# Kernel optimization log

Measured on AMD Instinct MI355X. Metric: run time of the kernel, lower is better.

## Reference

```python
import jax, jax.numpy as jnp
import numpy as np

NLAG = 300  # int(maxlag/dt) = int(3.0/0.01)


def setup_inputs() -> dict:
    key = jax.random.key(0)
    k1, k2 = jax.random.split(key)
    data1 = jax.random.normal(k1, (64, 32, 3000), dtype=jnp.float32)
    data2 = jax.random.normal(k2, (64, 32, 3000), dtype=jnp.float32)
    return {"data1": data1, "data2": data2}


def reference(data1, data2):
    # Time-domain full cross-correlation via grouped conv1d (PyTorch conv1d
    # does correlation, no kernel flip; lax.conv_general_dilated matches).
    nb, nc, nt = data1.shape
    g = nb * nc
    lhs = data1.reshape(1, g, nt)          # (N=1, C=g, T)
    rhs = data2.reshape(g, 1, nt)          # (O=g, I=1, T) one filter per group
    xcor = jax.lax.conv_general_dilated(
        lhs, rhs,
        window_strides=(1,),
        padding=[(NLAG + 1, NLAG + 1)],
        feature_group_count=g,
        dimension_numbers=("NCH", "OIH", "NCH"),
    )  # (1, g, 2*NLAG+3)
    return xcor.reshape(nb, nc, -1)
```

## Files before the change

### kernel.cpp

```cpp
#include <hip/hip_runtime.h>


#define NT    3000
#define NOUT  603
#define BLOCK 64
#define L1DW  1696
#define L2DW  2048

typedef short bf16x8 __attribute__((ext_vector_type(8)));
typedef float f32x4  __attribute__((ext_vector_type(4)));

static __device__ __forceinline__ uint f2bf(float f) {
    union { float f; uint u; } a; a.f = f;
    return (a.u + 0x7fffu + ((a.u >> 16) & 1u)) >> 16;
}

struct AFrag { uint m1, d0, d1, d2, d3; };

__global__ __launch_bounds__(BLOCK, 2) void xcorr_mfma(
    const float* __restrict__ d1g, const float* __restrict__ d2g,
    float* __restrict__ out)
{
    __shared__ __align__(16) uint l1[L1DW];
    __shared__ __align__(16) uint l2[L2DW];

    const int lane = threadIdx.x & 63;
    const int q = lane >> 4, r = lane & 15;
    const int ch = blockIdx.x;
    const float* __restrict__ g1 = d1g + (size_t)ch * NT;
    const float* __restrict__ g2 = d2g + (size_t)ch * NT;

    for (int j = lane; j < 196; j += BLOCK) {
        const int dw = (j < 152) ? j : 1652 + (j - 152);
        l1[dw] = 0u;
    }
    for (int j = lane; j < 548; j += BLOCK) {
        const int dw = (j < 384) ? j : 1884 + (j - 384);
        l2[dw] = 0u;
    }

    auto stageA = [&](int dstart) {
        const int d = dstart + 4 * lane;
        const int e0 = 2 * (d - 152);
        if (e0 < NT) {
            const float4 v = *(const float4*)(g1 + e0);
            const float4 w = *(const float4*)(g1 + e0 + 4);
            int4 p;
            p.x = (int)(f2bf(v.x) | (f2bf(v.y) << 16));
            p.y = (int)(f2bf(v.z) | (f2bf(v.w) << 16));
            p.z = (int)(f2bf(w.x) | (f2bf(w.y) << 16));
            p.w = (int)(f2bf(w.z) | (f2bf(w.w) << 16));
            *(int4*)(l1 + d) = p;
        }
    };
    auto stageB = [&](int dstart) {
        const int d = dstart + 4 * lane;
        const int e0 = 2 * (d - 384);
        if (e0 < NT) {
            const float4 v = *(const float4*)(g2 + e0);
            const float4 w = *(const float4*)(g2 + e0 + 4);
            int4 p;
            p.x = (int)(f2bf(v.x) | (f2bf(v.y) << 16));
            p.y = (int)(f2bf(v.z) | (f2bf(v.w) << 16));
            p.z = (int)(f2bf(w.x) | (f2bf(w.y) << 16));
            p.w = (int)(f2bf(w.z) | (f2bf(w.w) << 16));
            *(int4*)(l2 + d) = p;
        }
    };

    stageA(152); stageA(408);
    stageB(384); stageB(640);

    int4 fifo[16];
    {
        const int dbP = 256 + 4 * q - 16 * r;
        #pragma unroll
        for (int s = 0; s < 16; ++s)
            fifo[s] = *(const int4*)(l2 + dbP + 16 * s);
    }

    f32x4 a00 = {0.f,0.f,0.f,0.f};
    f32x4 a10 = {0.f,0.f,0.f,0.f};
    f32x4 a01 = {0.f,0.f,0.f,0.f};
    f32x4 a11 = {0.f,0.f,0.f,0.f};

    int da = 130 + 4 * q + r;
    int db = 512 + 4 * q - 16 * r;
    int aPre = 664, bPre = 896;

    auto ldsFetch = [&](int daL, int dbL, AFrag& A, int4& B) {
        const uint* pa = (const uint*)l1 + daL;
        A.m1 = pa[-1]; A.d0 = pa[0]; A.d1 = pa[1]; A.d2 = pa[2]; A.d3 = pa[3];
        B = *(const int4*)((const uint*)l2 + dbL);
    };

    AFrag curA; int4 curB;
    ldsFetch(da, db, curA, curB);
    AFrag nxtA = curA; int4 nxtB = curB;

    for (int c = 0; c < 6; ++c) {
        const int dA = aPre + 4 * lane, eA = 2 * (dA - 152);
        const int dB = bPre + 4 * lane, eB = 2 * (dB - 384);
        const bool okA = eA < NT, okB = eB < NT;
        float4 va0, va1, vb0, vb1;
        if (okA) { va0 = *(const float4*)(g1 + eA); va1 = *(const float4*)(g1 + eA + 4); }
        if (okB) { vb0 = *(const float4*)(g2 + eB); vb1 = *(const float4*)(g2 + eB + 4); }

        #pragma unroll
        for (int u = 0; u < 16; ++u) {
            if (u < 15 || c < 5)
                ldsFetch(da + 16, db + 16, nxtA, nxtB);

            union { uint w[4]; bf16x8 v; int4 i4; } f1, f0, g0, g1u;
            f1.w[0] = curA.d0; f1.w[1] = curA.d1;
            f1.w[2] = curA.d2; f1.w[3] = curA.d3;
            f0.w[0] = (curA.m1 >> 16) | (curA.d0 << 16);
            f0.w[1] = (curA.d0 >> 16) | (curA.d1 << 16);
            f0.w[2] = (curA.d1 >> 16) | (curA.d2 << 16);
            f0.w[3] = (curA.d2 >> 16) | (curA.d3 << 16);

            g0.i4  = curB;
            g1u.i4 = fifo[u];
            fifo[u] = g0.i4;

            a00 = __builtin_amdgcn_mfma_f32_16x16x32_bf16(f0.v, g0.v,  a00, 0, 0, 0);
            a10 = __builtin_amdgcn_mfma_f32_16x16x32_bf16(f1.v, g0.v,  a10, 0, 0, 0);
            a01 = __builtin_amdgcn_mfma_f32_16x16x32_bf16(f0.v, g1u.v, a01, 0, 0, 0);
            a11 = __builtin_amdgcn_mfma_f32_16x16x32_bf16(f1.v, g1u.v, a11, 0, 0, 0);

            curA = nxtA; curB = nxtB;
            da += 16; db += 16;
        }

        if (okA) {
            int4 p;
            p.x = (int)(f2bf(va0.x) | (f2bf(va0.y) << 16));
            p.y = (int)(f2bf(va0.z) | (f2bf(va0.w) << 16));
            p.z = (int)(f2bf(va1.x) | (f2bf(va1.y) << 16));
            p.w = (int)(f2bf(va1.z) | (f2bf(va1.w) << 16));
            *(int4*)(l1 + dA) = p;
        }
        if (okB) {
            int4 p;
            p.x = (int)(f2bf(vb0.x) | (f2bf(vb0.y) << 16));
            p.y = (int)(f2bf(vb0.z) | (f2bf(vb0.w) << 16));
            p.z = (int)(f2bf(vb1.x) | (f2bf(vb1.y) << 16));
            p.w = (int)(f2bf(vb1.z) | (f2bf(vb1.w) << 16));
            *(int4*)(l2 + dB) = p;
        }
        aPre += 256; bPre += 256;
    }

    float* o = out + (size_t)ch * NOUT;
    {
        const int X = 32 * r + 8 * q;
        float4 s0 = {a00[0], a10[0], a00[1], a10[1]};
        float4 s1 = {a00[2], a10[2], a00[3], a10[3]};
        *(float4*)(o + X)     = s0;
        *(float4*)(o + X + 4) = s1;
    }
    {
        const int X = 512 + 32 * r + 8 * q;
        if (X + 7 < NOUT) {
            float4 s0 = {a01[0], a11[0], a01[1], a11[1]};
            float4 s1 = {a01[2], a11[2], a01[3], a11[3]};
            *(float4*)(o + X)     = s0;
            *(float4*)(o + X + 4) = s1;
        } else if (X < NOUT) {
            const float v[8] = {a01[0], a11[0], a01[1], a11[1],
                                a01[2], a11[2], a01[3], a11[3]};
            #pragma unroll
            for (int e = 0; e < 8; ++e)
                if (X + e < NOUT) o[X + e] = v[e];
        }
    }
}

extern "C" void kernel_launch(void* const* d_in, const int* in_sizes, int n_in,
                              void* d_out, int out_size, void* d_ws, size_t ws_size,
                              hipStream_t stream) {
    const float* d1 = (const float*)d_in[0];
    const float* d2 = (const float*)d_in[1];
    float* out = (float*)d_out;
    const int nChannels = in_sizes[0] / NT;
    xcorr_mfma<<<nChannels, BLOCK, 0, stream>>>(d1, d2, out);
}
```

Baseline: 21.89 us.

## Process two channels per wave and prefetch next channel's prologue during compute

Each single-wave block now handles two channels in sequence, cutting the grid from 2048 to 1024 blocks. While the last chunks of the current channel are computing, it loads the next channel's first 1024 samples of both inputs and stages them into LDS regions that have already been consumed. This hides the per-channel prologue load latency behind MFMA work. In exchange there is less block-level parallelism, more registers are live, and the code assumes the channel count is even.

```diff
diff --git a/kernel.cpp b/kernel.cpp
--- a/kernel.cpp
+++ b/kernel.cpp
@@ -4,6 +4,7 @@
 #define NT    3000
 #define NOUT  603
 #define BLOCK 64
+#define CHPW  2
 #define L1DW  1696
 #define L2DW  2048
 
@@ -13,6 +14,15 @@
 static __device__ __forceinline__ uint f2bf(float f) {
     union { float f; uint u; } a; a.f = f;
     return (a.u + 0x7fffu + ((a.u >> 16) & 1u)) >> 16;
+}
+
+static __device__ __forceinline__ int4 pack8(float4 v, float4 w) {
+    int4 p;
+    p.x = (int)(f2bf(v.x) | (f2bf(v.y) << 16));
+    p.y = (int)(f2bf(v.z) | (f2bf(v.w) << 16));
+    p.z = (int)(f2bf(w.x) | (f2bf(w.y) << 16));
+    p.w = (int)(f2bf(w.z) | (f2bf(w.w) << 16));
+    return p;
 }
 
 struct AFrag { uint m1, d0, d1, d2, d3; };
@@ -26,9 +36,7 @@
 
     const int lane = threadIdx.x & 63;
     const int q = lane >> 4, r = lane & 15;
-    const int ch = blockIdx.x;
-    const float* __restrict__ g1 = d1g + (size_t)ch * NT;
-    const float* __restrict__ g2 = d2g + (size_t)ch * NT;
+    const int ch0 = blockIdx.x * CHPW;
 
     for (int j = lane; j < 196; j += BLOCK) {
         const int dw = (j < 152) ? j : 1652 + (j - 152);
@@ -39,140 +47,150 @@
         l2[dw] = 0u;
     }
 
-    auto stageA = [&](int dstart) {
-        const int d = dstart + 4 * lane;
-        const int e0 = 2 * (d - 152);
-        if (e0 < NT) {
-            const float4 v = *(const float4*)(g1 + e0);
-            const float4 w = *(const float4*)(g1 + e0 + 4);
-            int4 p;
-            p.x = (int)(f2bf(v.x) | (f2bf(v.y) << 16));
-            p.y = (int)(f2bf(v.z) | (f2bf(v.w) << 16));
-            p.z = (int)(f2bf(w.x) | (f2bf(w.y) << 16));
-            p.w = (int)(f2bf(w.z) | (f2bf(w.w) << 16));
-            *(int4*)(l1 + d) = p;
-        }
-    };
-    auto stageB = [&](int dstart) {
-        const int d = dstart + 4 * lane;
-        const int e0 = 2 * (d - 384);
-        if (e0 < NT) {
-            const float4 v = *(const float4*)(g2 + e0);
-            const float4 w = *(const float4*)(g2 + e0 + 4);
-            int4 p;
-            p.x = (int)(f2bf(v.x) | (f2bf(v.y) << 16));
-            p.y = (int)(f2bf(v.z) | (f2bf(v.w) << 16));
-            p.z = (int)(f2bf(w.x) | (f2bf(w.y) << 16));
-            p.w = (int)(f2bf(w.z) | (f2bf(w.w) << 16));
-            *(int4*)(l2 + d) = p;
-        }
-    };
-
-    stageA(152); stageA(408);
-    stageB(384); stageB(640);
-
-    int4 fifo[16];
+    const float* g1 = d1g + (size_t)ch0 * NT;
+    const float* g2 = d2g + (size_t)ch0 * NT;
+
     {
-        const int dbP = 256 + 4 * q - 16 * r;
-        #pragma unroll
-        for (int s = 0; s < 16; ++s)
-            fifo[s] = *(const int4*)(l2 + dbP + 16 * s);
-    }
-
-    f32x4 a00 = {0.f,0.f,0.f,0.f};
-    f32x4 a10 = {0.f,0.f,0.f,0.f};
-    f32x4 a01 = {0.f,0.f,0.f,0.f};
-    f32x4 a11 = {0.f,0.f,0.f,0.f};
-
-    int da = 130 + 4 * q + r;
-    int db = 512 + 4 * q - 16 * r;
-    int aPre = 664, bPre = 896;
-
-    auto ldsFetch = [&](int daL, int dbL, AFrag& A, int4& B) {
-        const uint* pa = (const uint*)l1 + daL;
-        A.m1 = pa[-1]; A.d0 = pa[0]; A.d1 = pa[1]; A.d2 = pa[2]; A.d3 = pa[3];
-        B = *(const int4*)((const uint*)l2 + dbL);
-    };
-
-    AFrag curA; int4 curB;
-    ldsFetch(da, db, curA, curB);
-    AFrag nxtA = curA; int4 nxtB = curB;
-
-    for (int c = 0; c < 6; ++c) {
-        const int dA = aPre + 4 * lane, eA = 2 * (dA - 152);
-        const int dB = bPre + 4 * lane, eB = 2 * (dB - 384);
-        const bool okA = eA < NT, okB = eB < NT;
-        float4 va0, va1, vb0, vb1;
-        if (okA) { va0 = *(const float4*)(g1 + eA); va1 = *(const float4*)(g1 + eA + 4); }
-        if (okB) { vb0 = *(const float4*)(g2 + eB); vb1 = *(const float4*)(g2 + eB + 4); }
-
-        #pragma unroll
-        for (int u = 0; u < 16; ++u) {
-            if (u < 15 || c < 5)
-                ldsFetch(da + 16, db + 16, nxtA, nxtB);
-
-            union { uint w[4]; bf16x8 v; int4 i4; } f1, f0, g0, g1u;
-            f1.w[0] = curA.d0; f1.w[1] = curA.d1;
-            f1.w[2] = curA.d2; f1.w[3] = curA.d3;
-            f0.w[0] = (curA.m1 >> 16) | (curA.d0 << 16);
-            f0.w[1] = (curA.d0 >> 16) | (curA.d1 << 16);
-            f0.w[2] = (curA.d1 >> 16) | (curA.d2 << 16);
-            f0.w[3] = (curA.d2 >> 16) | (curA.d3 << 16);
-
-            g0.i4  = curB;
-            g1u.i4 = fifo[u];
-            fifo[u] = g0.i4;
-
-            a00 = __builtin_amdgcn_mfma_f32_16x16x32_bf16(f0.v, g0.v,  a00, 0, 0, 0);
-            a10 = __builtin_amdgcn_mfma_f32_16x16x32_bf16(f1.v, g0.v,  a10, 0, 0, 0);
-            a01 = __builtin_amdgcn_mfma_f32_16x16x32_bf16(f0.v, g1u.v, a01, 0, 0, 0);
-            a11 = __builtin_amdgcn_mfma_f32_16x16x32_bf16(f1.v, g1u.v, a11, 0, 0, 0);
-
-            curA = nxtA; curB = nxtB;
-            da += 16; db += 16;
-        }
-
-        if (okA) {
-            int4 p;
-            p.x = (int)(f2bf(va0.x) | (f2bf(va0.y) << 16));
-            p.y = (int)(f2bf(va0.z) | (f2bf(va0.w) << 16));
-            p.z = (int)(f2bf(va1.x) | (f2bf(va1.y) << 16));
-            p.w = (int)(f2bf(va1.z) | (f2bf(va1.w) << 16));
-            *(int4*)(l1 + dA) = p;
-        }
-        if (okB) {
-            int4 p;
-            p.x = (int)(f2bf(vb0.x) | (f2bf(vb0.y) << 16));
-            p.y = (int)(f2bf(vb0.z) | (f2bf(vb0.w) << 16));
-            p.z = (int)(f2bf(vb1.x) | (f2bf(vb1.y) << 16));
-            p.w = (int)(f2bf(vb1.z) | (f2bf(vb1.w) << 16));
-            *(int4*)(l2 + dB) = p;
-        }
-        aPre += 256; bPre += 256;
-    }
-
-    float* o = out + (size_t)ch * NOUT;
-    {
-        const int X = 32 * r + 8 * q;
-        float4 s0 = {a00[0], a10[0], a00[1], a10[1]};
-        float4 s1 = {a00[2], a10[2], a00[3], a10[3]};
-        *(float4*)(o + X)     = s0;
-        *(float4*)(o + X + 4) = s1;
-    }
-    {
-        const int X = 512 + 32 * r + 8 * q;
-        if (X + 7 < NOUT) {
-            float4 s0 = {a01[0], a11[0], a01[1], a11[1]};
-            float4 s1 = {a01[2], a11[2], a01[3], a11[3]};
+        const int d = 4 * lane;
+        float4 v0 = *(const float4*)(g1 + 2 * d);
+        float4 v1 = *(const float4*)(g1 + 2 * d + 4);
+        *(int4*)(l1 + 152 + d) = pack8(v0, v1);
+        v0 = *(const float4*)(g1 + 512 + 2 * d);
+        v1 = *(const float4*)(g1 + 512 + 2 * d + 4);
+        *(int4*)(l1 + 408 + d) = pack8(v0, v1);
+        v0 = *(const float4*)(g2 + 2 * d);
+        v1 = *(const float4*)(g2 + 2 * d + 4);
+        *(int4*)(l2 + 384 + d) = pack8(v0, v1);
+        v0 = *(const float4*)(g2 + 512 + 2 * d);
+        v1 = *(const float4*)(g2 + 512 + 2 * d + 4);
+        *(int4*)(l2 + 640 + d) = pack8(v0, v1);
+    }
+
+    for (int cc = 0; cc < CHPW; ++cc) {
+        const bool notlast = (cc + 1 < CHPW);
+        const float* gn1 = g1 + NT;
+        const float* gn2 = g2 + NT;
+
+        int4 fifo[16];
+        {
+            const int dbP = 256 + 4 * q - 16 * r;
+            #pragma unroll
+            for (int s = 0; s < 16; ++s)
+                fifo[s] = *(const int4*)(l2 + dbP + 16 * s);
+        }
+
+        f32x4 a00 = {0.f,0.f,0.f,0.f};
+        f32x4 a10 = {0.f,0.f,0.f,0.f};
+        f32x4 a01 = {0.f,0.f,0.f,0.f};
+        f32x4 a11 = {0.f,0.f,0.f,0.f};
+
+        int da = 130 + 4 * q + r;
+        int db = 512 + 4 * q - 16 * r;
+        int aPre = 664, bPre = 896;
+
+        auto ldsFetch = [&](int daL, int dbL, AFrag& A, int4& B) {
+            const uint* pa = (const uint*)l1 + daL;
+            A.m1 = pa[-1]; A.d0 = pa[0]; A.d1 = pa[1]; A.d2 = pa[2]; A.d3 = pa[3];
+            B = *(const int4*)((const uint*)l2 + dbL);
+        };
+
+        AFrag curA; int4 curB;
+        ldsFetch(da, db, curA, curB);
+        AFrag nxtA = curA; int4 nxtB = curB;
+
+        float4 h0, h1, h2, h3;
+
+        for (int c = 0; c < 6; ++c) {
+            const int dA = aPre + 4 * lane, eA = 2 * (dA - 152);
+            const int dB = bPre + 4 * lane, eB = 2 * (dB - 384);
+            const bool okA = eA < NT, okB = eB < NT;
+            float4 va0, va1, vb0, vb1;
+            if (okA) { va0 = *(const float4*)(g1 + eA); va1 = *(const float4*)(g1 + eA + 4); }
+            if (okB) { vb0 = *(const float4*)(g2 + eB); vb1 = *(const float4*)(g2 + eB + 4); }
+
+            if (notlast && c == 4) {
+                const int d = 4 * lane;
+                h0 = *(const float4*)(gn1 + 2 * d);
+                h1 = *(const float4*)(gn1 + 2 * d + 4);
+                h2 = *(const float4*)(gn1 + 512 + 2 * d);
+                h3 = *(const float4*)(gn1 + 512 + 2 * d + 4);
+            }
+            if (notlast && c == 5) {
+                const int d = 4 * lane;
+                h0 = *(const float4*)(gn2 + 2 * d);
+                h1 = *(const float4*)(gn2 + 2 * d + 4);
+                h2 = *(const float4*)(gn2 + 512 + 2 * d);
+                h3 = *(const float4*)(gn2 + 512 + 2 * d + 4);
+            }
+
+            #pragma unroll
+            for (int u = 0; u < 16; ++u) {
+                if (u < 15 || c < 5)
+                    ldsFetch(da + 16, db + 16, nxtA, nxtB);
+
+                union { uint w[4]; bf16x8 v; int4 i4; } f1, f0, g0, g1u;
+                f1.w[0] = curA.d0; f1.w[1] = curA.d1;
+                f1.w[2] = curA.d2; f1.w[3] = curA.d3;
+                f0.w[0] = (curA.m1 >> 16) | (curA.d0 << 16);
+                f0.w[1] = (curA.d0 >> 16) | (curA.d1 << 16);
+                f0.w[2] = (curA.d1 >> 16) | (curA.d2 << 16);
+                f0.w[3] = (curA.d2 >> 16) | (curA.d3 << 16);
+
+                g0.i4  = curB;
+                g1u.i4 = fifo[u];
+                fifo[u] = g0.i4;
+
+                a00 = __builtin_amdgcn_mfma_f32_16x16x32_bf16(f0.v, g0.v,  a00, 0, 0, 0);
+                a10 = __builtin_amdgcn_mfma_f32_16x16x32_bf16(f1.v, g0.v,  a10, 0, 0, 0);
+                a01 = __builtin_amdgcn_mfma_f32_16x16x32_bf16(f0.v, g1u.v, a01, 0, 0, 0);
+                a11 = __builtin_amdgcn_mfma_f32_16x16x32_bf16(f1.v, g1u.v, a11, 0, 0, 0);
+
+                curA = nxtA; curB = nxtB;
+                da += 16; db += 16;
+            }
+
+            if (okA) *(int4*)(l1 + dA) = pack8(va0, va1);
+            if (okB) *(int4*)(l2 + dB) = pack8(vb0, vb1);
+
+            if (notlast && c == 4) {
+                const int d = 4 * lane;
+                *(int4*)(l1 + 152 + d) = pack8(h0, h1);
+                *(int4*)(l1 + 408 + d) = pack8(h2, h3);
+            }
+            if (notlast && c == 5) {
+                const int d = 4 * lane;
+                *(int4*)(l2 + 384 + d) = pack8(h0, h1);
+                *(int4*)(l2 + 640 + d) = pack8(h2, h3);
+            }
+
+            aPre += 256; bPre += 256;
+        }
+
+        float* o = out + (size_t)(ch0 + cc) * NOUT;
+        {
+            const int X = 32 * r + 8 * q;
+            float4 s0 = {a00[0], a10[0], a00[1], a10[1]};
+            float4 s1 = {a00[2], a10[2], a00[3], a10[3]};
             *(float4*)(o + X)     = s0;
             *(float4*)(o + X + 4) = s1;
-        } else if (X < NOUT) {
-            const float v[8] = {a01[0], a11[0], a01[1], a11[1],
-                                a01[2], a11[2], a01[3], a11[3]};
-            #pragma unroll
-            for (int e = 0; e < 8; ++e)
-                if (X + e < NOUT) o[X + e] = v[e];
-        }
+        }
+        {
+            const int X = 512 + 32 * r + 8 * q;
+            if (X + 7 < NOUT) {
+                float4 s0 = {a01[0], a11[0], a01[1], a11[1]};
+                float4 s1 = {a01[2], a11[2], a01[3], a11[3]};
+                *(float4*)(o + X)     = s0;
+                *(float4*)(o + X + 4) = s1;
+            } else if (X < NOUT) {
+                const float v[8] = {a01[0], a11[0], a01[1], a11[1],
+                                    a01[2], a11[2], a01[3], a11[3]};
+                #pragma unroll
+                for (int e = 0; e < 8; ++e)
+                    if (X + e < NOUT) o[X + e] = v[e];
+            }
+        }
+
+        g1 = gn1; g2 = gn2;
     }
 }
 
@@ -183,5 +201,6 @@
     const float* d2 = (const float*)d_in[1];
     float* out = (float*)d_out;
     const int nChannels = in_sizes[0] / NT;
-    xcorr_mfma<<<nChannels, BLOCK, 0, stream>>>(d1, d2, out);
-}
+    const int grid = nChannels / CHPW;
+    xcorr_mfma<<<grid, BLOCK, 0, stream>>>(d1, d2, out);
+}
```

Result: slower. 28.91 us (+32.1%).
